# Kernel tuning notes

Measured on AMD Instinct MI355X. Metric: run time of the kernel, lower is better.

Reference implementation:

```python
import jax, jax.numpy as jnp
import numpy as np

N_NODES = 50000
N_EDGES = 800000
DIM = 64


def setup_inputs() -> dict:
    key = jax.random.key(0)
    ks = jax.random.split(key, 11)
    d = DIM
    node_embeddings = jax.random.normal(ks[0], (N_NODES, d), dtype=jnp.float32)
    neighbour_attributes = jax.random.normal(ks[1], (N_EDGES, d), dtype=jnp.float32)
    batch_index = jnp.sort(jax.random.randint(ks[2], (N_EDGES,), 0, N_NODES))
    s_align = 1.0 / np.sqrt(2 * d)
    s_d = 1.0 / np.sqrt(d)
    # alignment_layer: Linear(2d -> 1)
    align_w = jax.random.uniform(ks[3], (1, 2 * d), jnp.float32, -s_align, s_align)
    align_b = jax.random.uniform(ks[4], (1,), jnp.float32, -s_align, s_align)
    # context_layer: Linear(d -> d)
    ctx_w = jax.random.uniform(ks[5], (d, d), jnp.float32, -s_d, s_d)
    ctx_b = jax.random.uniform(ks[6], (d,), jnp.float32, -s_d, s_d)
    # readout_layer: GRUCell(d, d) -- torch layout [3d, d] gates (r, z, n)
    w_ih = jax.random.uniform(ks[7], (3 * d, d), jnp.float32, -s_d, s_d)
    w_hh = jax.random.uniform(ks[8], (3 * d, d), jnp.float32, -s_d, s_d)
    b_ih = jax.random.uniform(ks[9], (3 * d,), jnp.float32, -s_d, s_d)
    b_hh = jax.random.uniform(ks[10], (3 * d,), jnp.float32, -s_d, s_d)
    return {
        "node_embeddings": node_embeddings,
        "neighbour_attributes": neighbour_attributes,
        "batch_index": batch_index,
        "align_w": align_w, "align_b": align_b,
        "ctx_w": ctx_w, "ctx_b": ctx_b,
        "w_ih": w_ih, "w_hh": w_hh, "b_ih": b_ih, "b_hh": b_hh,
    }


def reference(node_embeddings, neighbour_attributes, batch_index,
              align_w, align_b, ctx_w, ctx_b, w_ih, w_hh, b_ih, b_hh):
    n = node_embeddings.shape[0]
    # _expand_and_join: gather node row per edge, concat with neighbour feats -> [E, 2d]
    joint = jnp.concatenate([node_embeddings[batch_index], neighbour_attributes], axis=1)
    # alignment + leaky_relu (torch default negative_slope=0.01); dropout is identity (p=0)
    scores = jax.nn.leaky_relu(joint @ align_w.T + align_b, negative_slope=0.01)[:, 0]  # [E]
    # segment softmax over variable-size neighbourhoods (torch_geometric softmax)
    seg_max = jax.ops.segment_max(scores, batch_index, num_segments=n)
    seg_max = jnp.where(jnp.isfinite(seg_max), seg_max, 0.0)  # guard empty segments
    ex = jnp.exp(scores - jax.lax.stop_gradient(seg_max)[batch_index])
    denom = jax.ops.segment_sum(ex, batch_index, num_segments=n)[batch_index]
    attn = (ex / jnp.maximum(denom, 1e-16))[:, None]  # [E, 1]
    # attention-weighted context messages, scatter-add pooled per node, then ELU
    msgs = attn * (neighbour_attributes @ ctx_w.T + ctx_b)  # [E, d]
    contexts = jax.nn.elu(jax.ops.segment_sum(msgs, batch_index, num_segments=n))  # [N, d]
    # GRUCell(contexts, node_embeddings), torch gate order (r, z, n)
    gi = contexts @ w_ih.T + b_ih
    gh = node_embeddings @ w_hh.T + b_hh
    i_r, i_z, i_n = jnp.split(gi, 3, axis=1)
    h_r, h_z, h_n = jnp.split(gh, 3, axis=1)
    r = jax.nn.sigmoid(i_r + h_r)
    z = jax.nn.sigmoid(i_z + h_z)
    g = jnp.tanh(i_n + r * h_n)
    h_new = (1.0 - z) * g + z * node_embeddings
    return jax.nn.relu(h_new)
```

## Files before the change

### kernel.cpp

```cpp
#include <hip/hip_runtime.h>
#include <stdint.h>

constexpr int kN = 50000;
constexpr int kE = 800000;
constexpr int kD = 64;

typedef short sv8 __attribute__((ext_vector_type(8)));
typedef float fv4 __attribute__((ext_vector_type(4)));

__device__ __forceinline__ float bf2f(uint16_t u) {
    union { uint32_t i; float f; } v; v.i = ((uint32_t)u) << 16; return v.f;
}
__device__ __forceinline__ uint16_t f2bf(float f) {
    union { float ff; uint32_t i; } v; v.ff = f;
    return (uint16_t)((v.i + 0x7FFFu + ((v.i >> 16) & 1u)) >> 16);
}
__device__ __forceinline__ float wsum64(float x) {
    x += __shfl_xor(x, 1);  x += __shfl_xor(x, 2);  x += __shfl_xor(x, 4);
    x += __shfl_xor(x, 8);  x += __shfl_xor(x, 16); x += __shfl_xor(x, 32);
    return x;
}

template<int BF> __device__ __forceinline__ float ldf(const void* p, int i) {
    if (BF) return bf2f(((const uint16_t*)p)[i]);
    return ((const float*)p)[i];
}
template<int BF> __device__ __forceinline__ void stf(void* p, int i, float v) {
    if (BF) ((uint16_t*)p)[i] = f2bf(v);
    else    ((float*)p)[i] = v;
}
template<int BF> __device__ __forceinline__ sv8 ldfrag(const void* p, int elem_base) {
    if (BF) {
        return *(const sv8*)((const uint16_t*)p + elem_base);
    } else {
        const float* f = (const float*)p + elem_base;
        sv8 r;
#pragma unroll
        for (int i = 0; i < 8; ++i) r[i] = (short)f2bf(f[i]);
        return r;
    }
}
__device__ __forceinline__ fv4 mfma16(sv8 a, sv8 b, fv4 c) {
    return __builtin_amdgcn_mfma_f32_16x16x32_bf16(a, b, c, 0, 0, 0);
}

__global__ void k_prep(const int* __restrict__ bi, int* __restrict__ rp,
                       const uint16_t* __restrict__ nbr, int* __restrict__ flag) {
    if (blockIdx.x == gridDim.x - 1) {
        int lane = threadIdx.x;
        if (lane < 64) {
            float an = 0.f;
            for (int i = lane; i < 512; i += 64) {
                uint16_t u = nbr[i];
                if ((u & 0x7fffu) != 0) {
                    float a = fabsf(bf2f(u));
                    if (!(a >= 1e-8f && a <= 1e8f)) an += 1.f;
                }
            }
            an = wsum64(an);
            if (lane == 0) flag[0] = (an > 0.5f) ? 0 : 1;
        }
        return;
    }
    int n = blockIdx.x * 256 + threadIdx.x;
    if (n > kN) return;
    int lo = 0, hi = kE;
    while (lo < hi) { int mid = (lo + hi) >> 1; if (bi[mid] < n) lo = mid + 1; else hi = mid; }
    rp[n] = lo;
}

template<int BF>
__device__ __forceinline__ void edges_body(
    const void* node_emb, const void* nbr, const void* align_w, const void* align_b,
    const int* rp, uint16_t* weighted, float* fhas)
{
    const int lane = threadIdx.x & 63;
    const int n    = blockIdx.x * 4 + (threadIdx.x >> 6);
    const int g    = lane >> 4;
    const int t    = lane & 15;

    float nd = wsum64(ldf<BF>(node_emb, n * kD + lane) * ldf<BF>(align_w, lane))
             + ldf<BF>(align_b, 0);

    float w0 = ldf<BF>(align_w, kD + t * 4 + 0);
    float w1 = ldf<BF>(align_w, kD + t * 4 + 1);
    float w2 = ldf<BF>(align_w, kD + t * 4 + 2);
    float w3 = ldf<BF>(align_w, kD + t * 4 + 3);

    const int s0 = rp[n], s1 = rp[n + 1];
    float l = 0.f;
    float a0 = 0.f, a1 = 0.f, a2 = 0.f, a3 = 0.f;

    for (int eb = s0; eb < s1; eb += 4) {
        int e = eb + g;
        bool valid = (e < s1);
        int ec = valid ? e : s0;
        float v0, v1, v2, v3;
        if (BF) {
            uint2 u = *(const uint2*)((const uint16_t*)nbr + ec * kD + t * 4);
            v0 = bf2f((uint16_t)u.x); v1 = bf2f((uint16_t)(u.x >> 16));
            v2 = bf2f((uint16_t)u.y); v3 = bf2f((uint16_t)(u.y >> 16));
        } else {
            float4 f = *(const float4*)((const float*)nbr + ec * kD + t * 4);
            v0 = f.x; v1 = f.y; v2 = f.z; v3 = f.w;
        }
        float part = v0 * w0 + v1 * w1 + v2 * w2 + v3 * w3;
        part += __shfl_xor(part, 1);
        part += __shfl_xor(part, 2);
        part += __shfl_xor(part, 4);
        part += __shfl_xor(part, 8);
        float s = part + nd;
        s = (s > 0.f) ? s : 0.01f * s;
        float p = valid ? __expf(s) : 0.f;
        l  += p;
        a0 += p * v0;
        a1 += p * v1;
        a2 += p * v2;
        a3 += p * v3;
    }

    l  += __shfl_xor(l, 16);   l  += __shfl_xor(l, 32);
    a0 += __shfl_xor(a0, 16);  a0 += __shfl_xor(a0, 32);
    a1 += __shfl_xor(a1, 16);  a1 += __shfl_xor(a1, 32);
    a2 += __shfl_xor(a2, 16);  a2 += __shfl_xor(a2, 32);
    a3 += __shfl_xor(a3, 16);  a3 += __shfl_xor(a3, 32);

    if (g == 0) {
        float inv = (s1 > s0) ? (1.f / l) : 0.f;
        uint32_t lo = (uint32_t)f2bf(a0 * inv) | ((uint32_t)f2bf(a1 * inv) << 16);
        uint32_t hi = (uint32_t)f2bf(a2 * inv) | ((uint32_t)f2bf(a3 * inv) << 16);
        *(uint2*)(weighted + n * kD + t * 4) = make_uint2(lo, hi);
        if (t == 0) fhas[n] = (s1 > s0) ? 1.f : 0.f;
    }
}
__global__ __launch_bounds__(256, 4) void k_edges(
    const void* node_emb, const void* nbr, const void* aw, const void* ab,
    const int* __restrict__ rp, const int* __restrict__ flag,
    uint16_t* __restrict__ weighted, float* __restrict__ fhas)
{
    if (*flag) edges_body<1>(node_emb, nbr, aw, ab, rp, weighted, fhas);
    else       edges_body<0>(node_emb, nbr, aw, ab, rp, weighted, fhas);
}

template<int BF>
__device__ __forceinline__ void gru_body(
    const void* node_emb,
    const void* ctx_w, const void* ctx_b,
    const void* w_ih,  const void* w_hh,
    const void* b_ih,  const void* b_hh,
    const uint16_t* weighted, const float* fhas, void* out,
    uint16_t* swt,
    uint16_t (*sctx)[16][72])
{
    const int tid  = threadIdx.x;
    const int lane = tid & 63;
    const int wv   = tid >> 6;
    const int R    = blockIdx.x * 64 + wv * 16;
    const int t    = lane & 15;
    const int q    = lane >> 4;

    const fv4 zf = {0.f, 0.f, 0.f, 0.f};

    {
        const void* srcs[2] = { w_ih, w_hh };
#pragma unroll
        for (int hlf = 0; hlf < 2; ++hlf) {
            const void* src = srcs[hlf];
            uint16_t* dst = swt + hlf * 192 * 72;
            for (int off = tid * 8; off < 192 * 64; off += 256 * 8) {
                int r = off >> 6, c = off & 63;
                if (BF) {
                    *(uint4*)(dst + r * 72 + c) =
                        *(const uint4*)((const uint16_t*)src + off);
                } else {
                    const float* f = (const float*)src + off;
                    uint32_t p0 = (uint32_t)f2bf(f[0]) | ((uint32_t)f2bf(f[1]) << 16);
                    uint32_t p1 = (uint32_t)f2bf(f[2]) | ((uint32_t)f2bf(f[3]) << 16);
                    uint32_t p2 = (uint32_t)f2bf(f[4]) | ((uint32_t)f2bf(f[5]) << 16);
                    uint32_t p3 = (uint32_t)f2bf(f[6]) | ((uint32_t)f2bf(f[7]) << 16);
                    *(uint4*)(dst + r * 72 + c) = make_uint4(p0, p1, p2, p3);
                }
            }
        }
    }

    int ar = R + t; if (ar > kN - 1) ar = kN - 1;
    sv8 ah0 = ldfrag<BF>(node_emb, ar * kD + q * 8);
    sv8 ah1 = ldfrag<BF>(node_emb, ar * kD + q * 8 + 32);
    sv8 aw0 = ldfrag<1>(weighted, ar * kD + q * 8);
    sv8 aw1 = ldfrag<1>(weighted, ar * kD + q * 8 + 32);

    __syncthreads();

    fv4 accC[4];
#pragma unroll
    for (int ct = 0; ct < 4; ++ct) {
        int rb = (ct * 16 + t) * kD + q * 8;
        fv4 a = zf;
        a = mfma16(aw0, ldfrag<BF>(ctx_w, rb),      a);
        a = mfma16(aw1, ldfrag<BF>(ctx_w, rb + 32), a);
        accC[ct] = a;
    }

    float has_i[4];
#pragma unroll
    for (int i = 0; i < 4; ++i) {
        int node = R + q * 4 + i; if (node > kN - 1) node = kN - 1;
        has_i[i] = fhas[node];
    }
#pragma unroll
    for (int ct = 0; ct < 4; ++ct) {
        int col = ct * 16 + t;
        float cb = ldf<BF>(ctx_b, col);
#pragma unroll
        for (int i = 0; i < 4; ++i) {
            float x = accC[ct][i] + has_i[i] * cb;
            x = (x > 0.f) ? x : (__expf(x) - 1.f);
            sctx[wv][q * 4 + i][col] = f2bf(x);
        }
    }
    __syncthreads();

    sv8 ac0 = *(const sv8*)&sctx[wv][t][q * 8];
    sv8 ac1 = *(const sv8*)&sctx[wv][t][q * 8 + 32];

    const uint16_t* ih = swt;
    const uint16_t* hh = swt + 192 * 72;

#pragma unroll
    for (int jt = 0; jt < 4; ++jt) {
        const int rr = jt * 16 + t;
        fv4 air = zf, aiz = zf, ain = zf, ahr = zf, ahz = zf, ahn = zf;
        air = mfma16(ac0, *(const sv8*)&ih[ rr        * 72 + q * 8],      air);
        air = mfma16(ac1, *(const sv8*)&ih[ rr        * 72 + q * 8 + 32], air);
        aiz = mfma16(ac0, *(const sv8*)&ih[(rr +  64) * 72 + q * 8],      aiz);
        aiz = mfma16(ac1, *(const sv8*)&ih[(rr +  64) * 72 + q * 8 + 32], aiz);
        ain = mfma16(ac0, *(const sv8*)&ih[(rr + 128) * 72 + q * 8],      ain);
        ain = mfma16(ac1, *(const sv8*)&ih[(rr + 128) * 72 + q * 8 + 32], ain);
        ahr = mfma16(ah0, *(const sv8*)&hh[ rr        * 72 + q * 8],      ahr);
        ahr = mfma16(ah1, *(const sv8*)&hh[ rr        * 72 + q * 8 + 32], ahr);
        ahz = mfma16(ah0, *(const sv8*)&hh[(rr +  64) * 72 + q * 8],      ahz);
        ahz = mfma16(ah1, *(const sv8*)&hh[(rr +  64) * 72 + q * 8 + 32], ahz);
        ahn = mfma16(ah0, *(const sv8*)&hh[(rr + 128) * 72 + q * 8],      ahn);
        ahn = mfma16(ah1, *(const sv8*)&hh[(rr + 128) * 72 + q * 8 + 32], ahn);

        const int col = jt * 16 + t;
        float bir = ldf<BF>(b_ih, col),       bhr = ldf<BF>(b_hh, col);
        float biz = ldf<BF>(b_ih, 64 + col),  bhz = ldf<BF>(b_hh, 64 + col);
        float bin = ldf<BF>(b_ih, 128 + col), bhn = ldf<BF>(b_hh, 128 + col);
#pragma unroll
        for (int i = 0; i < 4; ++i) {
            int node = R + q * 4 + i;
            bool valid = node < kN;
            int cn = valid ? node : kN - 1;
            float hv = ldf<BF>(node_emb, cn * kD + col);
            float r = 1.f / (1.f + __expf(-(air[i] + bir + ahr[i] + bhr)));
            float z = 1.f / (1.f + __expf(-(aiz[i] + biz + ahz[i] + bhz)));
            float tt = ain[i] + bin + r * (ahn[i] + bhn);
            float gg = 2.f / (1.f + __expf(-2.f * tt)) - 1.f;
            float hn = (1.f - z) * gg + z * hv;
            if (valid) stf<BF>(out, node * kD + col, fmaxf(hn, 0.f));
        }
    }
}
__global__ __launch_bounds__(256, 2) void k_gru(
    const void* node_emb, const void* ctx_w, const void* ctx_b,
    const void* w_ih, const void* w_hh, const void* b_ih, const void* b_hh,
    const uint16_t* __restrict__ weighted, const float* __restrict__ fhas,
    const int* __restrict__ flag, void* out)
{
    __shared__ uint16_t swt[384 * 72];
    __shared__ uint16_t sctx[4][16][72];
    if (*flag) gru_body<1>(node_emb, ctx_w, ctx_b, w_ih, w_hh, b_ih, b_hh, weighted, fhas, out, swt, sctx);
    else       gru_body<0>(node_emb, ctx_w, ctx_b, w_ih, w_hh, b_ih, b_hh, weighted, fhas, out, swt, sctx);
}

extern "C" void kernel_launch(void* const* d_in, const int* in_sizes, int n_in,
                              void* d_out, int out_size, void* d_ws, size_t ws_size,
                              hipStream_t stream) {
    (void)in_sizes; (void)n_in; (void)out_size; (void)ws_size;
    const void* node_emb = d_in[0];
    const void* nbr      = d_in[1];
    const int*  bi       = (const int*)d_in[2];
    const void* align_w  = d_in[3];
    const void* align_b  = d_in[4];
    const void* ctx_w    = d_in[5];
    const void* ctx_b    = d_in[6];
    const void* w_ih     = d_in[7];
    const void* w_hh     = d_in[8];
    const void* b_ih     = d_in[9];
    const void* b_hh     = d_in[10];

    char* ws = (char*)d_ws;
    int*      row_ptr  = (int*)ws;
    int*      flag     = (int*)(ws + 200064);
    float*    fhas     = (float*)(ws + 204800);
    uint16_t* weighted = (uint16_t*)(ws + 409600);

    k_prep<<<(kN + 256) / 256 + 1, 256, 0, stream>>>(bi, row_ptr, (const uint16_t*)nbr, flag);
    k_edges<<<kN / 4, 256, 0, stream>>>(node_emb, nbr, align_w, align_b, row_ptr, flag, weighted, fhas);
    k_gru<<<(kN + 63) / 64, 256, 0, stream>>>(node_emb, ctx_w, ctx_b, w_ih, w_hh, b_ih, b_hh,
                                              weighted, fhas, flag, d_out);
}
```

Baseline: 349.4 us.

## Fuse row-pointer search into edge kernel and map one node per quarter-wave

After: 360.5 us. 3.2% more time.

```diff
diff --git a/kernel.cpp b/kernel.cpp
--- a/kernel.cpp
+++ b/kernel.cpp
@@ -44,64 +44,86 @@
     return __builtin_amdgcn_mfma_f32_16x16x32_bf16(a, b, c, 0, 0, 0);
 }
 
-__global__ void k_prep(const int* __restrict__ bi, int* __restrict__ rp,
-                       const uint16_t* __restrict__ nbr, int* __restrict__ flag) {
-    if (blockIdx.x == gridDim.x - 1) {
-        int lane = threadIdx.x;
-        if (lane < 64) {
-            float an = 0.f;
-            for (int i = lane; i < 512; i += 64) {
-                uint16_t u = nbr[i];
-                if ((u & 0x7fffu) != 0) {
-                    float a = fabsf(bf2f(u));
-                    if (!(a >= 1e-8f && a <= 1e8f)) an += 1.f;
-                }
+__device__ __forceinline__ int detect_bf16(const uint16_t* __restrict__ nbr) {
+    const int lane = threadIdx.x & 63;
+    uint4 v = ((const uint4*)nbr)[lane];
+    uint32_t w[4] = { v.x, v.y, v.z, v.w };
+    float an = 0.f;
+#pragma unroll
+    for (int k = 0; k < 4; ++k) {
+#pragma unroll
+        for (int h = 0; h < 2; ++h) {
+            uint16_t u = (uint16_t)(w[k] >> (16 * h));
+            if ((u & 0x7fffu) != 0) {
+                float a = fabsf(bf2f(u));
+                if (!(a >= 1e-8f && a <= 1e8f)) an += 1.f;
             }
-            an = wsum64(an);
-            if (lane == 0) flag[0] = (an > 0.5f) ? 0 : 1;
-        }
-        return;
-    }
-    int n = blockIdx.x * 256 + threadIdx.x;
-    if (n > kN) return;
-    int lo = 0, hi = kE;
-    while (lo < hi) { int mid = (lo + hi) >> 1; if (bi[mid] < n) lo = mid + 1; else hi = mid; }
-    rp[n] = lo;
+        }
+    }
+    an = wsum64(an);
+    return (an > 0.5f) ? 0 : 1;
 }
 
 template<int BF>
 __device__ __forceinline__ void edges_body(
     const void* node_emb, const void* nbr, const void* align_w, const void* align_b,
-    const int* rp, uint16_t* weighted, float* fhas)
+    const int* __restrict__ bi, uint16_t* weighted, float* fhas)
 {
     const int lane = threadIdx.x & 63;
-    const int n    = blockIdx.x * 4 + (threadIdx.x >> 6);
+    const int wv   = threadIdx.x >> 6;
+    const int nb   = blockIdx.x * 16 + wv * 4;
     const int g    = lane >> 4;
     const int t    = lane & 15;
-
-    float nd = wsum64(ldf<BF>(node_emb, n * kD + lane) * ldf<BF>(align_w, lane))
-             + ldf<BF>(align_b, 0);
+    const int n    = nb + g;
+
+    float nd;
+    {
+        float p0, p1, p2, p3, u0, u1, u2, u3;
+        if (BF) {
+            uint2 a = *(const uint2*)((const uint16_t*)node_emb + n * kD + t * 4);
+            uint2 w = *(const uint2*)((const uint16_t*)align_w + t * 4);
+            p0 = bf2f((uint16_t)a.x); p1 = bf2f((uint16_t)(a.x >> 16));
+            p2 = bf2f((uint16_t)a.y); p3 = bf2f((uint16_t)(a.y >> 16));
+            u0 = bf2f((uint16_t)w.x); u1 = bf2f((uint16_t)(w.x >> 16));
+            u2 = bf2f((uint16_t)w.y); u3 = bf2f((uint16_t)(w.y >> 16));
+        } else {
+            float4 a = *(const float4*)((const float*)node_emb + n * kD + t * 4);
+            float4 w = *(const float4*)((const float*)align_w + t * 4);
+            p0 = a.x; p1 = a.y; p2 = a.z; p3 = a.w;
+            u0 = w.x; u1 = w.y; u2 = w.z; u3 = w.w;
+        }
+        float d = p0 * u0 + p1 * u1 + p2 * u2 + p3 * u3;
+        d += __shfl_xor(d, 1); d += __shfl_xor(d, 2);
+        d += __shfl_xor(d, 4); d += __shfl_xor(d, 8);
+        nd = d + ldf<BF>(align_b, 0);
+    }
 
     float w0 = ldf<BF>(align_w, kD + t * 4 + 0);
     float w1 = ldf<BF>(align_w, kD + t * 4 + 1);
     float w2 = ldf<BF>(align_w, kD + t * 4 + 2);
     float w3 = ldf<BF>(align_w, kD + t * 4 + 3);
 
-    const int s0 = rp[n], s1 = rp[n + 1];
-    float l = 0.f;
-    float a0 = 0.f, a1 = 0.f, a2 = 0.f, a3 = 0.f;
-
-    for (int eb = s0; eb < s1; eb += 4) {
-        int e = eb + g;
-        bool valid = (e < s1);
-        int ec = valid ? e : s0;
+    int lo;
+    {
+        const int ns = nb + (lane < 5 ? lane : 4);
+        lo = 0; int hi = kE;
+        int gl = ns * 16 - 2048, gh = ns * 16 + 2048;
+        if (gl > 0 && gl < kE && bi[gl] < ns)  lo = gl;
+        if (gh > 0 && gh < kE && bi[gh] >= ns) hi = gh;
+        while (lo < hi) { int mid = (lo + hi) >> 1; if (bi[mid] < ns) lo = mid + 1; else hi = mid; }
+    }
+    const int s0 = __shfl(lo, g);
+    const int s1 = __shfl(lo, g + 1);
+
+    float l = 0.f, a0 = 0.f, a1 = 0.f, a2 = 0.f, a3 = 0.f;
+    for (int e = s0; e < s1; ++e) {
         float v0, v1, v2, v3;
         if (BF) {
-            uint2 u = *(const uint2*)((const uint16_t*)nbr + ec * kD + t * 4);
+            uint2 u = *(const uint2*)((const uint16_t*)nbr + (size_t)e * kD + t * 4);
             v0 = bf2f((uint16_t)u.x); v1 = bf2f((uint16_t)(u.x >> 16));
             v2 = bf2f((uint16_t)u.y); v3 = bf2f((uint16_t)(u.y >> 16));
         } else {
-            float4 f = *(const float4*)((const float*)nbr + ec * kD + t * 4);
+            float4 f = *(const float4*)((const float*)nbr + (size_t)e * kD + t * 4);
             v0 = f.x; v1 = f.y; v2 = f.z; v3 = f.w;
         }
         float part = v0 * w0 + v1 * w1 + v2 * w2 + v3 * w3;
@@ -111,7 +133,7 @@
         part += __shfl_xor(part, 8);
         float s = part + nd;
         s = (s > 0.f) ? s : 0.01f * s;
-        float p = valid ? __expf(s) : 0.f;
+        float p = __expf(s);
         l  += p;
         a0 += p * v0;
         a1 += p * v1;
@@ -119,27 +141,20 @@
         a3 += p * v3;
     }
 
-    l  += __shfl_xor(l, 16);   l  += __shfl_xor(l, 32);
-    a0 += __shfl_xor(a0, 16);  a0 += __shfl_xor(a0, 32);
-    a1 += __shfl_xor(a1, 16);  a1 += __shfl_xor(a1, 32);
-    a2 += __shfl_xor(a2, 16);  a2 += __shfl_xor(a2, 32);
-    a3 += __shfl_xor(a3, 16);  a3 += __shfl_xor(a3, 32);
-
-    if (g == 0) {
-        float inv = (s1 > s0) ? (1.f / l) : 0.f;
-        uint32_t lo = (uint32_t)f2bf(a0 * inv) | ((uint32_t)f2bf(a1 * inv) << 16);
-        uint32_t hi = (uint32_t)f2bf(a2 * inv) | ((uint32_t)f2bf(a3 * inv) << 16);
-        *(uint2*)(weighted + n * kD + t * 4) = make_uint2(lo, hi);
-        if (t == 0) fhas[n] = (s1 > s0) ? 1.f : 0.f;
-    }
+    float inv = (s1 > s0) ? (1.f / l) : 0.f;
+    uint32_t plo = (uint32_t)f2bf(a0 * inv) | ((uint32_t)f2bf(a1 * inv) << 16);
+    uint32_t phi = (uint32_t)f2bf(a2 * inv) | ((uint32_t)f2bf(a3 * inv) << 16);
+    *(uint2*)(weighted + (size_t)n * kD + t * 4) = make_uint2(plo, phi);
+    if (t == 0) fhas[n] = (s1 > s0) ? 1.f : 0.f;
 }
 __global__ __launch_bounds__(256, 4) void k_edges(
     const void* node_emb, const void* nbr, const void* aw, const void* ab,
-    const int* __restrict__ rp, const int* __restrict__ flag,
+    const int* __restrict__ bi,
     uint16_t* __restrict__ weighted, float* __restrict__ fhas)
 {
-    if (*flag) edges_body<1>(node_emb, nbr, aw, ab, rp, weighted, fhas);
-    else       edges_body<0>(node_emb, nbr, aw, ab, rp, weighted, fhas);
+    const int flag = detect_bf16((const uint16_t*)nbr);
+    if (flag) edges_body<1>(node_emb, nbr, aw, ab, bi, weighted, fhas);
+    else      edges_body<0>(node_emb, nbr, aw, ab, bi, weighted, fhas);
 }
 
 template<int BF>
@@ -267,12 +282,13 @@
     const void* node_emb, const void* ctx_w, const void* ctx_b,
     const void* w_ih, const void* w_hh, const void* b_ih, const void* b_hh,
     const uint16_t* __restrict__ weighted, const float* __restrict__ fhas,
-    const int* __restrict__ flag, void* out)
+    const uint16_t* __restrict__ nbr, void* out)
 {
     __shared__ uint16_t swt[384 * 72];
     __shared__ uint16_t sctx[4][16][72];
-    if (*flag) gru_body<1>(node_emb, ctx_w, ctx_b, w_ih, w_hh, b_ih, b_hh, weighted, fhas, out, swt, sctx);
-    else       gru_body<0>(node_emb, ctx_w, ctx_b, w_ih, w_hh, b_ih, b_hh, weighted, fhas, out, swt, sctx);
+    const int flag = detect_bf16(nbr);
+    if (flag) gru_body<1>(node_emb, ctx_w, ctx_b, w_ih, w_hh, b_ih, b_hh, weighted, fhas, out, swt, sctx);
+    else      gru_body<0>(node_emb, ctx_w, ctx_b, w_ih, w_hh, b_ih, b_hh, weighted, fhas, out, swt, sctx);
 }
 
 extern "C" void kernel_launch(void* const* d_in, const int* in_sizes, int n_in,
@@ -292,13 +308,10 @@
     const void* b_hh     = d_in[10];
 
     char* ws = (char*)d_ws;
-    int*      row_ptr  = (int*)ws;
-    int*      flag     = (int*)(ws + 200064);
-    float*    fhas     = (float*)(ws + 204800);
-    uint16_t* weighted = (uint16_t*)(ws + 409600);
-
-    k_prep<<<(kN + 256) / 256 + 1, 256, 0, stream>>>(bi, row_ptr, (const uint16_t*)nbr, flag);
-    k_edges<<<kN / 4, 256, 0, stream>>>(node_emb, nbr, align_w, align_b, row_ptr, flag, weighted, fhas);
+    float*    fhas     = (float*)ws;
+    uint16_t* weighted = (uint16_t*)(ws + 204800);
+
+    k_edges<<<kN / 16, 256, 0, stream>>>(node_emb, nbr, align_w, align_b, bi, weighted, fhas);
     k_gru<<<(kN + 63) / 64, 256, 0, stream>>>(node_emb, ctx_w, ctx_b, w_ih, w_hh, b_ih, b_hh,
-                                              weighted, fhas, flag, d_out);
-}
+                                              weighted, fhas, (const uint16_t*)nbr, d_out);
+}
```

## Assign one node per 16-lane group in edge kernel and narrow row-pointer search

Applied to the files above, without the earlier changes.

Result: no change. 355.5 us (+1.8%).

```diff
diff --git a/kernel.cpp b/kernel.cpp
--- a/kernel.cpp
+++ b/kernel.cpp
@@ -65,6 +65,9 @@
     int n = blockIdx.x * 256 + threadIdx.x;
     if (n > kN) return;
     int lo = 0, hi = kE;
+    int gl = n * 16 - 2048, gh = n * 16 + 2048;
+    if (gl > 0 && gl < kE && bi[gl] < n)  lo = gl;
+    if (gh > 0 && gh < kE && bi[gh] >= n) hi = gh;
     while (lo < hi) { int mid = (lo + hi) >> 1; if (bi[mid] < n) lo = mid + 1; else hi = mid; }
     rp[n] = lo;
 }
@@ -72,36 +75,53 @@
 template<int BF>
 __device__ __forceinline__ void edges_body(
     const void* node_emb, const void* nbr, const void* align_w, const void* align_b,
-    const int* rp, uint16_t* weighted, float* fhas)
+    const int* __restrict__ rp, uint16_t* weighted, float* fhas)
 {
     const int lane = threadIdx.x & 63;
-    const int n    = blockIdx.x * 4 + (threadIdx.x >> 6);
+    const int wv   = threadIdx.x >> 6;
+    const int nb   = blockIdx.x * 16 + wv * 4;
     const int g    = lane >> 4;
     const int t    = lane & 15;
-
-    float nd = wsum64(ldf<BF>(node_emb, n * kD + lane) * ldf<BF>(align_w, lane))
-             + ldf<BF>(align_b, 0);
+    const int n    = nb + g;
+
+    const int s0 = rp[n], s1 = rp[n + 1];
+
+    float nd;
+    {
+        float p0, p1, p2, p3, u0, u1, u2, u3;
+        if (BF) {
+            uint2 a = *(const uint2*)((const uint16_t*)node_emb + n * kD + t * 4);
+            uint2 w = *(const uint2*)((const uint16_t*)align_w + t * 4);
+            p0 = bf2f((uint16_t)a.x); p1 = bf2f((uint16_t)(a.x >> 16));
+            p2 = bf2f((uint16_t)a.y); p3 = bf2f((uint16_t)(a.y >> 16));
+            u0 = bf2f((uint16_t)w.x); u1 = bf2f((uint16_t)(w.x >> 16));
+            u2 = bf2f((uint16_t)w.y); u3 = bf2f((uint16_t)(w.y >> 16));
+        } else {
+            float4 a = *(const float4*)((const float*)node_emb + n * kD + t * 4);
+            float4 w = *(const float4*)((const float*)align_w + t * 4);
+            p0 = a.x; p1 = a.y; p2 = a.z; p3 = a.w;
+            u0 = w.x; u1 = w.y; u2 = w.z; u3 = w.w;
+        }
+        float d = p0 * u0 + p1 * u1 + p2 * u2 + p3 * u3;
+        d += __shfl_xor(d, 1); d += __shfl_xor(d, 2);
+        d += __shfl_xor(d, 4); d += __shfl_xor(d, 8);
+        nd = d + ldf<BF>(align_b, 0);
+    }
 
     float w0 = ldf<BF>(align_w, kD + t * 4 + 0);
     float w1 = ldf<BF>(align_w, kD + t * 4 + 1);
     float w2 = ldf<BF>(align_w, kD + t * 4 + 2);
     float w3 = ldf<BF>(align_w, kD + t * 4 + 3);
 
-    const int s0 = rp[n], s1 = rp[n + 1];
-    float l = 0.f;
-    float a0 = 0.f, a1 = 0.f, a2 = 0.f, a3 = 0.f;
-
-    for (int eb = s0; eb < s1; eb += 4) {
-        int e = eb + g;
-        bool valid = (e < s1);
-        int ec = valid ? e : s0;
+    float l = 0.f, a0 = 0.f, a1 = 0.f, a2 = 0.f, a3 = 0.f;
+    for (int e = s0; e < s1; ++e) {
         float v0, v1, v2, v3;
         if (BF) {
-            uint2 u = *(const uint2*)((const uint16_t*)nbr + ec * kD + t * 4);
+            uint2 u = *(const uint2*)((const uint16_t*)nbr + (size_t)e * kD + t * 4);
             v0 = bf2f((uint16_t)u.x); v1 = bf2f((uint16_t)(u.x >> 16));
             v2 = bf2f((uint16_t)u.y); v3 = bf2f((uint16_t)(u.y >> 16));
         } else {
-            float4 f = *(const float4*)((const float*)nbr + ec * kD + t * 4);
+            float4 f = *(const float4*)((const float*)nbr + (size_t)e * kD + t * 4);
             v0 = f.x; v1 = f.y; v2 = f.z; v3 = f.w;
         }
         float part = v0 * w0 + v1 * w1 + v2 * w2 + v3 * w3;
@@ -111,7 +131,7 @@
         part += __shfl_xor(part, 8);
         float s = part + nd;
         s = (s > 0.f) ? s : 0.01f * s;
-        float p = valid ? __expf(s) : 0.f;
+        float p = __expf(s);
         l  += p;
         a0 += p * v0;
         a1 += p * v1;
@@ -119,19 +139,11 @@
         a3 += p * v3;
     }
 
-    l  += __shfl_xor(l, 16);   l  += __shfl_xor(l, 32);
-    a0 += __shfl_xor(a0, 16);  a0 += __shfl_xor(a0, 32);
-    a1 += __shfl_xor(a1, 16);  a1 += __shfl_xor(a1, 32);
-    a2 += __shfl_xor(a2, 16);  a2 += __shfl_xor(a2, 32);
-    a3 += __shfl_xor(a3, 16);  a3 += __shfl_xor(a3, 32);
-
-    if (g == 0) {
-        float inv = (s1 > s0) ? (1.f / l) : 0.f;
-        uint32_t lo = (uint32_t)f2bf(a0 * inv) | ((uint32_t)f2bf(a1 * inv) << 16);
-        uint32_t hi = (uint32_t)f2bf(a2 * inv) | ((uint32_t)f2bf(a3 * inv) << 16);
-        *(uint2*)(weighted + n * kD + t * 4) = make_uint2(lo, hi);
-        if (t == 0) fhas[n] = (s1 > s0) ? 1.f : 0.f;
-    }
+    float inv = (s1 > s0) ? (1.f / l) : 0.f;
+    uint32_t plo = (uint32_t)f2bf(a0 * inv) | ((uint32_t)f2bf(a1 * inv) << 16);
+    uint32_t phi = (uint32_t)f2bf(a2 * inv) | ((uint32_t)f2bf(a3 * inv) << 16);
+    *(uint2*)(weighted + (size_t)n * kD + t * 4) = make_uint2(plo, phi);
+    if (t == 0) fhas[n] = (s1 > s0) ? 1.f : 0.f;
 }
 __global__ __launch_bounds__(256, 4) void k_edges(
     const void* node_emb, const void* nbr, const void* aw, const void* ab,
@@ -298,7 +310,7 @@
     uint16_t* weighted = (uint16_t*)(ws + 409600);
 
     k_prep<<<(kN + 256) / 256 + 1, 256, 0, stream>>>(bi, row_ptr, (const uint16_t*)nbr, flag);
-    k_edges<<<kN / 4, 256, 0, stream>>>(node_emb, nbr, align_w, align_b, row_ptr, flag, weighted, fhas);
+    k_edges<<<kN / 16, 256, 0, stream>>>(node_emb, nbr, align_w, align_b, row_ptr, flag, weighted, fhas);
     k_gru<<<(kN + 63) / 64, 256, 0, stream>>>(node_emb, ctx_w, ctx_b, w_ih, w_hh, b_ih, b_hh,
                                               weighted, fhas, flag, d_out);
 }
```
